# Kernel optimization log

Hardware: AMD Instinct MI355X
Metric: run time of the kernel (lower is better)

Reference implementation:

```python
import jax, jax.numpy as jnp
import numpy as np

B, T, D = 2, 2048, 2048
H = 8
KEY_DIM, VAL_DIM = 1024, 2048   # expand_k=0.5, expand_v=1.0
HK, HV = KEY_DIM // H, VAL_DIM // H
LOW_RANK = 16
GATE_NORM = 16.0
CHUNK = 64
HIDDEN = (D * 4 * 2 // 3 + 63) // 64 * 64  # 5504, exactly as GLUFFN.__init__
EPS = 1e-6


def rmsnorm(x, w):
    return x * jax.lax.rsqrt(jnp.mean(x * x, axis=-1, keepdims=True) + EPS) * w


def setup_inputs() -> dict:
    key = jax.random.key(0)
    ks = jax.random.split(key, 12)
    w = lambda k, s: jax.random.normal(k, s, jnp.float32) * 0.02
    return {
        "x": jax.random.normal(ks[0], (B, T, D), jnp.float32),
        "norm1_w": jnp.ones((D,), jnp.float32),
        "wq": w(ks[1], (D, KEY_DIM)),
        "wk": w(ks[2], (D, KEY_DIM)),
        "wv": w(ks[3], (D, VAL_DIM)),
        "gk_w1": w(ks[4], (D, LOW_RANK)),
        "gk_w2": w(ks[5], (LOW_RANK, KEY_DIM)),
        "gk_b": jnp.zeros((KEY_DIM,), jnp.float32),
        "wg": w(ks[6], (D, VAL_DIM)),
        "gnorm_w": jnp.ones((HV,), jnp.float32),
        "wo": w(ks[7], (VAL_DIM, D)),
        "ffn_norm_w": jnp.ones((D,), jnp.float32),
        "w_gate": w(ks[8], (D, HIDDEN)),
        "w_up": w(ks[9], (D, HIDDEN)),
        "w_down": w(ks[10], (HIDDEN, D)),
    }


def _gla(h, wq, wk, wv, gk_w1, gk_w2, gk_b, wg, gnorm_w, wo):
    # Gated linear attention, chunk-parallel form (fla-style):
    #   S_t = diag(exp(g_t)) S_{t-1} + k_t^T v_t ;  o_t = q_t S_t
    Bb, Tt, _ = h.shape
    nc = Tt // CHUNK

    def split(t, hd):  # [B,T,H*hd] -> [nc,B,H,CHUNK,hd]
        t = t.reshape(Bb, nc, CHUNK, H, hd)
        return jnp.transpose(t, (1, 0, 3, 2, 4))

    q = split(h @ wq, HK) * (HK ** -0.5)
    k = split(h @ wk, HK)
    v = split(h @ wv, HV)
    # low-rank forget gate, log-sigmoid scaled by gate_logit_normalizer=16
    g = split(jax.nn.log_sigmoid(h @ gk_w1 @ gk_w2 + gk_b) / GATE_NORM, HK)

    mask = jnp.tril(jnp.ones((CHUNK, CHUNK), jnp.float32))

    def step(S, inp):
        qc, kc, vc, gc = inp                       # [B,H,C,*]
        b = jnp.cumsum(gc, axis=-2)                # cumulative log-decay within chunk
        qe = qc * jnp.exp(b)
        A = jnp.einsum('bhik,bhjk->bhij', qe, kc * jnp.exp(-b)) * mask
        o = jnp.einsum('bhck,bhkv->bhcv', qe, S) + jnp.einsum('bhij,bhjv->bhiv', A, vc)
        bl = b[:, :, -1:, :]                       # decay to end of chunk
        S = jnp.exp(bl[:, :, 0, :])[..., None] * S + \
            jnp.einsum('bhck,bhcv->bhkv', kc * jnp.exp(bl - b), vc)
        return S, o

    S0 = jnp.zeros((Bb, H, HK, HV), h.dtype)
    _, o = jax.lax.scan(step, S0, (q, k, v, g))    # o: [nc,B,H,C,HV]
    o = jnp.transpose(o, (1, 0, 3, 2, 4)).reshape(Bb, Tt, H, HV)

    gate = (h @ wg).reshape(Bb, Tt, H, HV)
    # per-head RMSNorm + swish output gate (FusedRMSNormSwishGate)
    o = rmsnorm(o, gnorm_w) * gate * jax.nn.sigmoid(gate)
    return o.reshape(Bb, Tt, VAL_DIM) @ wo


def reference(x, norm1_w, wq, wk, wv, gk_w1, gk_w2, gk_b, wg, gnorm_w, wo,
              ffn_norm_w, w_gate, w_up, w_down):
    h = rmsnorm(x, norm1_w)
    x = x + _gla(h, wq, wk, wv, gk_w1, gk_w2, gk_b, wg, gnorm_w, wo)
    h2 = rmsnorm(x, ffn_norm_w)
    ffn = (jax.nn.silu(h2 @ w_gate) * (h2 @ w_up)) @ w_down  # GLUFFN, dropout=eval
    return x + ffn
```

## Files before the change

kernel.cpp:

```cpp
#include <hip/hip_runtime.h>

typedef unsigned short u16;
typedef __attribute__((ext_vector_type(8))) short bh8;
typedef __attribute__((ext_vector_type(4))) float f4;

__device__ __forceinline__ float bf2f(u16 u) {
  union { unsigned int i; float f; } x; x.i = ((unsigned int)u) << 16; return x.f;
}
__device__ __forceinline__ u16 f2bf(float f) {
  union { float f; unsigned int i; } x; x.f = f;
  unsigned int r = x.i + 0x7fffu + ((x.i >> 16) & 1u);
  return (u16)(r >> 16);
}
__device__ __forceinline__ f4 mfma16(bh8 a, bh8 b, f4 c) {
  return __builtin_amdgcn_mfma_f32_16x16x32_bf16(a, b, c, 0, 0, 0);
}
__device__ __forceinline__ void gload16(const void* g, void* l) {
  __builtin_amdgcn_global_load_lds(
      (const __attribute__((address_space(1))) void*)g,
      (__attribute__((address_space(3))) void*)l, 16, 0, 0);
}

__device__ __forceinline__ bh8 rd8(const u16* arr, int row, int col, int rowbytes) {
  return *(const bh8*)((const char*)arr + row * rowbytes + ((col * 2) ^ ((row & 7) << 4)));
}

__global__ __launch_bounds__(256)
void wtrans_k(const float* __restrict__ src, u16* __restrict__ dst, int R, int C,
              int rmul, int roff) {
  __shared__ float tile[32][33];
  int tx = threadIdx.x & 31, ty = threadIdx.x >> 5;
  int c0 = blockIdx.x * 32, r0 = blockIdx.y * 32;
#pragma unroll
  for (int yy = 0; yy < 32; yy += 8)
    tile[ty + yy][tx] = src[(size_t)(r0 + ty + yy) * C + c0 + tx];
  __syncthreads();
#pragma unroll
  for (int yy = 0; yy < 32; yy += 8)
    dst[(size_t)((c0 + ty + yy) * rmul + roff) * R + r0 + tx] = f2bf(tile[tx][ty + yy]);
}

__global__ __launch_bounds__(256)
void rmsnorm_k(const float* __restrict__ x, const float* __restrict__ w,
               u16* __restrict__ out) {
  int row = blockIdx.x, t = threadIdx.x;
  const float* xr = x + (size_t)row * 2048;
  float4 a = ((const float4*)xr)[t * 2];
  float4 b = ((const float4*)xr)[t * 2 + 1];
  float ss = a.x*a.x + a.y*a.y + a.z*a.z + a.w*a.w
           + b.x*b.x + b.y*b.y + b.z*b.z + b.w*b.w;
#pragma unroll
  for (int s = 32; s > 0; s >>= 1) ss += __shfl_xor(ss, s, 64);
  __shared__ float red[4];
  if ((t & 63) == 0) red[t >> 6] = ss;
  __syncthreads();
  float rr = rsqrtf((red[0] + red[1] + red[2] + red[3]) * (1.0f / 2048.0f) + 1e-6f);
  float v[8] = {a.x, a.y, a.z, a.w, b.x, b.y, b.z, b.w};
  int c0 = t * 8;
  u16* orow = out + (size_t)row * 2048 + c0;
#pragma unroll
  for (int j = 0; j < 8; ++j) orow[j] = f2bf(v[j] * rr * w[c0 + j]);
}

template <int EPI, int BN, typename OutT>
__global__ __launch_bounds__(256, 2)
void gemm2(const u16* __restrict__ A, const u16* __restrict__ Bt,
           OutT* __restrict__ C, void* __restrict__ aux, float scale,
           int M, int N, int K, int gx) {
  constexpr int SB = (BN == 256) ? 24576 : 16384;
  constexpr int NBS = (BN == 256) ? 4 : 2;
  constexpr int MB = (BN == 256) ? 8 : 4;
  __shared__ char lds[3 * SB];
  int t = threadIdx.x, lane = t & 63, w = t >> 6;
  int c_ = lane & 15, r_ = lane >> 4;
  int wm = (BN == 256) ? 0 : (w >> 1);
  int wn = (BN == 256) ? w : (w & 1);

  int nwg = gridDim.x;
  int wg = (blockIdx.x & 7) * (nwg >> 3) + (blockIdx.x >> 3);
  int gy = nwg / gx;
  int bx = wg / gy, by = wg % gy;
  int m0 = by * 128, n0 = bx * BN;

  const char* baseA[2];
#pragma unroll
  for (int h = 0; h < 2; ++h) {
    int p = h * 256 + t;
    int cc = p ^ ((p >> 3) & 7);
    baseA[h] = (const char*)A + ((size_t)(m0 + (cc >> 2)) * K + (cc & 3) * 8) * 2;
  }
  const char* baseB[NBS];
#pragma unroll
  for (int s = 0; s < NBS; ++s) {
    int p = s * 256 + t;
    int cc = p ^ ((p >> 3) & 7);
    baseB[s] = (const char*)Bt + ((size_t)(n0 + (cc >> 2)) * K + (cc & 3) * 8) * 2;
  }
  int offA[MB], offB[4];
#pragma unroll
  for (int mb = 0; mb < MB; ++mb) {
    int cc = (wm * 64 + mb * 16 + c_) * 4 + r_;
    offA[mb] = (cc ^ ((cc >> 3) & 7)) * 16;
  }
#pragma unroll
  for (int nb = 0; nb < 4; ++nb) {
    int cc = (wn * 64 + nb * 16 + c_) * 4 + r_;
    offB[nb] = (cc ^ ((cc >> 3) & 7)) * 16 + 8192;
  }
  int ldsW = w * 1024;

  f4 z4 = {0.f, 0.f, 0.f, 0.f};
  f4 acc[MB][4];
#pragma unroll
  for (int mb = 0; mb < MB; ++mb)
#pragma unroll
    for (int nb = 0; nb < 4; ++nb) acc[mb][nb] = z4;

  int NT = K >> 5;

#define STAGE(S, ko)                                                        \
  {                                                                         \
    _Pragma("unroll") for (int h = 0; h < 2; ++h)                           \
        gload16(baseA[h] + (ko), lds + (S) * SB + h * 4096 + ldsW);         \
    _Pragma("unroll") for (int s = 0; s < NBS; ++s)                         \
        gload16(baseB[s] + (ko), lds + (S) * SB + 8192 + s * 4096 + ldsW);  \
  }
#define WAIT_VM()                                                           \
  if (BN == 256) { asm volatile("s_waitcnt vmcnt(6)" ::: "memory"); }       \
  else { asm volatile("s_waitcnt vmcnt(4)" ::: "memory"); }
#define KTILE(S)                                                            \
  {                                                                         \
    bh8 afr[MB], bfr[4];                                                    \
    _Pragma("unroll") for (int nb = 0; nb < 4; ++nb)                        \
        bfr[nb] = *(const bh8*)(lds + (S) * SB + offB[nb]);                 \
    _Pragma("unroll") for (int mb = 0; mb < MB; ++mb)                       \
        afr[mb] = *(const bh8*)(lds + (S) * SB + offA[mb]);                 \
    int kts = kt + 2; if (kts >= NT) kts -= NT;                             \
    STAGE(((S) + 2) % 3, kts << 6);                                         \
    WAIT_VM();                                                              \
    __builtin_amdgcn_s_barrier();                                           \
    asm volatile("s_waitcnt lgkmcnt(0)" ::: "memory");                      \
    __builtin_amdgcn_sched_barrier(0);                                      \
    __builtin_amdgcn_s_setprio(1);                                          \
    _Pragma("unroll") for (int mb = 0; mb < MB; ++mb)                       \
        _Pragma("unroll") for (int nb = 0; nb < 4; ++nb)                    \
            acc[mb][nb] = mfma16(afr[mb], bfr[nb], acc[mb][nb]);            \
    __builtin_amdgcn_s_setprio(0);                                          \
    __builtin_amdgcn_sched_barrier(0);                                      \
    __builtin_amdgcn_s_barrier();                                           \
    asm volatile("" ::: "memory");                                          \
  }

  STAGE(0, 0);
  STAGE(1, 64);
  WAIT_VM();
  __builtin_amdgcn_s_barrier();
  asm volatile("" ::: "memory");

  int kt = 0;
  while (true) {
    KTILE(0); if (++kt == NT) break;
    KTILE(1); if (++kt == NT) break;
    KTILE(2); if (++kt == NT) break;
  }
  asm volatile("s_waitcnt vmcnt(0)" ::: "memory");
#undef KTILE
#undef WAIT_VM
#undef STAGE

  int rowBase = m0 + wm * 64;
#pragma unroll
  for (int mb = 0; mb < MB; ++mb) {
#pragma unroll
    for (int rr = 0; rr < 4; ++rr) {
      int row = rowBase + mb * 16 + r_ * 4 + rr;
#pragma unroll
      for (int nb = 0; nb < 4; ++nb) {
        int col = n0 + wn * 64 + nb * 16 + c_;
        float val = acc[mb][nb][rr];
        if (EPI == 1) {
          ((float*)C)[(size_t)row * N + col] = val + ((const float*)aux)[(size_t)row * N + col];
        } else if (EPI == 5) {
          if (col < 1024) ((u16*)C)[(size_t)row * 1024 + col] = f2bf(val * scale);
          else ((u16*)aux)[(size_t)row * 1024 + col - 1024] = f2bf(val);
        } else if (EPI == 4) {
          if (col < 2048) {
            int bb = row >> 11, t2 = row & 2047;
            int pan = ((bb << 5) + (t2 >> 6)) * 8 + (col >> 8);
            int ii = t2 & 63, vv = col & 255;
            *(u16*)((char*)C + (size_t)pan * 32768 + vv * 128 + ((ii * 2) ^ ((vv & 7) << 4)))
                = f2bf(val);
          } else {
            ((u16*)aux)[(size_t)row * 2048 + col - 2048] = f2bf(val);
          }
        } else if (EPI == 6) {
          float other = __shfl_xor(val, 1, 64);
          if (lane & 1) {
            float gv = other;
            ((u16*)C)[(size_t)row * 5504 + (col >> 1)] = f2bf(val * (gv / (1.f + expf(-gv))));
          }
        }
      }
    }
  }
}

__global__ __launch_bounds__(256)
void lowrank_k(const u16* __restrict__ h, const float* __restrict__ w1,
               const float* __restrict__ w2, const float* __restrict__ bias,
               float* __restrict__ g) {
  int row = blockIdx.x, t = threadIdx.x, lane = t & 63, wave = t >> 6;
  const u16* hr = h + (size_t)row * 2048;
  bh8 hv = *(const bh8*)&hr[t * 8];
  float p[16];
#pragma unroll
  for (int j = 0; j < 16; ++j) p[j] = 0.f;
#pragma unroll
  for (int kk = 0; kk < 8; ++kk) {
    float f = bf2f((u16)hv[kk]);
    const float* wrow = w1 + (size_t)(t * 8 + kk) * 16;
#pragma unroll
    for (int j = 0; j < 16; ++j) p[j] += f * wrow[j];
  }
#pragma unroll
  for (int j = 0; j < 16; ++j)
#pragma unroll
    for (int s = 32; s > 0; s >>= 1) p[j] += __shfl_xor(p[j], s, 64);
  __shared__ float gl[4][16];
  if (lane == 0) {
#pragma unroll
    for (int j = 0; j < 16; ++j) gl[wave][j] = p[j];
  }
  __syncthreads();
  float glow[16];
#pragma unroll
  for (int j = 0; j < 16; ++j) glow[j] = gl[0][j] + gl[1][j] + gl[2][j] + gl[3][j];
  float* grow = g + (size_t)row * 1024;
#pragma unroll
  for (int nn = 0; nn < 4; ++nn) {
    int n = nn * 256 + t;
    float z = bias[n];
#pragma unroll
    for (int j = 0; j < 16; ++j) z += glow[j] * w2[j * 1024 + n];
    float ls = fminf(z, 0.f) - log1pf(expf(-fabsf(z)));
    grow[n] = ls * (1.0f / 16.0f);
  }
}

__global__ __launch_bounds__(128)
void gprep_k(u16* __restrict__ q, u16* __restrict__ k, const float* __restrict__ g,
             u16* __restrict__ keT, float* __restrict__ ebl) {
  int bid = blockIdx.x;
  int h = bid & 7, bc = bid >> 3;
  int b = bc >> 5, c = bc & 31;
  int ch = threadIdx.x;
  size_t base = ((size_t)(b * 2048 + c * 64)) * 1024 + h * 128 + ch;
  char* keTp = (char*)keT + (size_t)bid * 16384 + ch * 128;
  int sw = (ch & 7) << 4;
  float bacc = 0.f;
  for (int i8 = 0; i8 < 8; ++i8) {
    u16 kp[8];
#pragma unroll
    for (int e = 0; e < 8; ++e) {
      size_t off = base + (size_t)(i8 * 8 + e) * 1024;
      bacc += g[off];
      float eb = __expf(bacc);
      float reb = __builtin_amdgcn_rcpf(eb);
      float qv = bf2f(q[off]), kv = bf2f(k[off]);
      q[off] = f2bf(qv * eb);
      u16 kev = f2bf(kv * reb);
      k[off] = kev;
      kp[e] = kev;
    }
    *(bh8*)(keTp + ((i8 * 16) ^ sw)) = *(const bh8*)kp;
  }
  ebl[(size_t)bid * 128 + ch] = __expf(bacc);
}

__global__ __launch_bounds__(256)
void gla_scan(const u16* __restrict__ qg, const u16* __restrict__ kg,
              const u16* __restrict__ keTg, const u16* __restrict__ vTg,
              const float* __restrict__ eblg, float* __restrict__ outp) {
  __shared__ u16 qeL[64 * 128];
  __shared__ u16 keL[64 * 128];
  __shared__ u16 kTL[128 * 64];
  __shared__ u16 vTL[64 * 64];
  __shared__ u16 AL[64 * 64];
  __shared__ u16 SbL[64 * 128];
  __shared__ float SfL[64][133];

  int t = threadIdx.x, lane = t & 63, w = t >> 6;
  int vb = blockIdx.x & 3, bh = blockIdx.x >> 2;
  int b = bh >> 3, h = bh & 7;
  int c_ = lane & 15, r_ = lane >> 4;
  f4 z4 = {0.f, 0.f, 0.f, 0.f};

  for (int i = t; i < 64 * 128; i += 256) SbL[i] = 0;
  for (int i = t; i < 64 * 133; i += 256) ((float*)SfL)[i] = 0.f;

  const char* qbase = (const char*)qg + (size_t)b * 2048 * 2048 + h * 256;
  const char* kbase = (const char*)kg + (size_t)b * 2048 * 2048 + h * 256;
  int rowoff = (t >> 4) * 2048 + (t & 15) * 16;
  int4 pq[4], pk[4], pkt[4], pvt[2];

#define LOADCH(cc)                                                              \
  {                                                                             \
    const char* qc = qbase + (size_t)(cc) * 64 * 2048;                          \
    const char* kc = kbase + (size_t)(cc) * 64 * 2048;                          \
    int panel_ = ((b * 32 + (cc)) * 8 + h);                                     \
    const char* ktc = (const char*)keTg + (size_t)panel_ * 16384;               \
    const char* vtc = (const char*)vTg + (size_t)panel_ * 32768 + vb * 8192;    \
    _Pragma("unroll")                                                           \
    for (int j = 0; j < 4; ++j) {                                               \
      pq[j] = *(const int4*)(qc + j * 16 * 2048 + rowoff);                      \
      pk[j] = *(const int4*)(kc + j * 16 * 2048 + rowoff);                      \
      pkt[j] = *(const int4*)(ktc + j * 4096 + t * 16);                         \
    }                                                                           \
    _Pragma("unroll")                                                           \
    for (int j = 0; j < 2; ++j) pvt[j] = *(const int4*)(vtc + j * 4096 + t * 16); \
  }

  LOADCH(0);
  for (int c = 0; c < 32; ++c) {
#pragma unroll
    for (int j = 0; j < 4; ++j) {
      int L = j * 4096 + t * 16;
      int d = (L & ~255) | ((L & 255) ^ (((L >> 8) & 7) << 4));
      *(int4*)((char*)qeL + d) = pq[j];
      *(int4*)((char*)keL + d) = pk[j];
      *(int4*)((char*)kTL + L) = pkt[j];
    }
#pragma unroll
    for (int j = 0; j < 2; ++j) *(int4*)((char*)vTL + j * 4096 + t * 16) = pvt[j];
    if (c < 31) LOADCH(c + 1);
    int panel = ((b * 32 + c) * 8 + h);
    float eblr[2][4];
#pragma unroll
    for (int kt = 0; kt < 2; ++kt)
#pragma unroll
      for (int r = 0; r < 4; ++r)
        eblr[kt][r] = eblg[(size_t)panel * 128 + w * 32 + kt * 16 + r_ * 4 + r];
    __syncthreads();

    f4 accA[4] = {z4, z4, z4, z4};
    f4 accS[2][4] = {{z4, z4, z4, z4}, {z4, z4, z4, z4}};
#pragma unroll
    for (int ks = 0; ks < 4; ++ks) {
      bh8 a = rd8(qeL, w * 16 + c_, ks * 32 + r_ * 8, 256);
#pragma unroll
      for (int n = 0; n < 4; ++n)
        accA[n] = mfma16(a, rd8(keL, n * 16 + c_, ks * 32 + r_ * 8, 256), accA[n]);
    }
#pragma unroll
    for (int ks = 0; ks < 2; ++ks) {
      bh8 bf_[4];
#pragma unroll
      for (int n = 0; n < 4; ++n) bf_[n] = rd8(vTL, n * 16 + c_, ks * 32 + r_ * 8, 128);
#pragma unroll
      for (int kt = 0; kt < 2; ++kt) {
        bh8 a = rd8(kTL, w * 32 + kt * 16 + c_, ks * 32 + r_ * 8, 128);
#pragma unroll
        for (int n = 0; n < 4; ++n) accS[kt][n] = mfma16(a, bf_[n], accS[kt][n]);
      }
    }
#pragma unroll
    for (int n = 0; n < 4; ++n)
#pragma unroll
      for (int r = 0; r < 4; ++r) {
        int i = w * 16 + r_ * 4 + r, j = n * 16 + c_;
        *(u16*)((char*)AL + i * 128 + ((j * 2) ^ ((i & 7) << 4))) =
            (j <= i) ? f2bf(accA[n][r]) : (u16)0;
      }
    __syncthreads();

    f4 acco[4] = {z4, z4, z4, z4};
#pragma unroll
    for (int ks = 0; ks < 4; ++ks) {
      bh8 a = rd8(qeL, w * 16 + c_, ks * 32 + r_ * 8, 256);
#pragma unroll
      for (int n = 0; n < 4; ++n)
        acco[n] = mfma16(a, rd8(SbL, n * 16 + c_, ks * 32 + r_ * 8, 256), acco[n]);
    }
#pragma unroll
    for (int ks = 0; ks < 2; ++ks) {
      bh8 a = rd8(AL, w * 16 + c_, ks * 32 + r_ * 8, 128);
#pragma unroll
      for (int n = 0; n < 4; ++n)
        acco[n] = mfma16(a, rd8(vTL, n * 16 + c_, ks * 32 + r_ * 8, 128), acco[n]);
    }
    {
      size_t obase = (size_t)(b * 2048 + c * 64 + w * 16 + r_ * 4) * 2048 + h * 256 + vb * 64;
#pragma unroll
      for (int n = 0; n < 4; ++n)
#pragma unroll
        for (int r = 0; r < 4; ++r)
          outp[obase + (size_t)r * 2048 + n * 16 + c_] = acco[n][r];
    }
    __syncthreads();

#pragma unroll
    for (int kt = 0; kt < 2; ++kt)
#pragma unroll
      for (int n = 0; n < 4; ++n)
#pragma unroll
        for (int r = 0; r < 4; ++r) {
          int kk = w * 32 + kt * 16 + r_ * 4 + r;
          int vcol = n * 16 + c_;
          float nv = eblr[kt][r] * (SfL[vcol][kk] + accS[kt][n][r]);
          SfL[vcol][kk] = nv;
          *(u16*)((char*)SbL + vcol * 256 + ((kk * 2) ^ ((vcol & 7) << 4))) = f2bf(nv);
        }
    __syncthreads();
  }
#undef LOADCH
}

__global__ __launch_bounds__(256)
void ogate_k(const float* __restrict__ o, const u16* __restrict__ gate,
             const float* __restrict__ gw, u16* __restrict__ og) {
  int tok = blockIdx.x, t = threadIdx.x;
  int head = t >> 5, l32 = t & 31, v0 = l32 * 8;
  size_t base = (size_t)tok * 2048 + head * 256 + v0;
  float4 a = *(const float4*)&o[base];
  float4 b = *(const float4*)&o[base + 4];
  float ov[8] = {a.x, a.y, a.z, a.w, b.x, b.y, b.z, b.w};
  float ss = 0.f;
#pragma unroll
  for (int j = 0; j < 8; ++j) ss += ov[j] * ov[j];
#pragma unroll
  for (int s = 16; s > 0; s >>= 1) ss += __shfl_xor(ss, s, 32);
  float rr = rsqrtf(ss * (1.0f / 256.0f) + 1e-6f);
#pragma unroll
  for (int j = 0; j < 8; ++j) {
    float gv = bf2f(gate[base + j]);
    float val = ov[j] * rr * gw[v0 + j];
    og[base + j] = f2bf(val * gv / (1.f + expf(-gv)));
  }
}

extern "C" void kernel_launch(void* const* d_in, const int* in_sizes, int n_in,
                              void* d_out, int out_size, void* d_ws, size_t ws_size,
                              hipStream_t stream) {
  (void)in_sizes; (void)n_in; (void)out_size; (void)ws_size;
  const float* x = (const float*)d_in[0];
  const float* n1w = (const float*)d_in[1];
  const float* wq = (const float*)d_in[2];
  const float* wk = (const float*)d_in[3];
  const float* wv = (const float*)d_in[4];
  const float* gw1 = (const float*)d_in[5];
  const float* gw2 = (const float*)d_in[6];
  const float* gb = (const float*)d_in[7];
  const float* wg = (const float*)d_in[8];
  const float* gnw = (const float*)d_in[9];
  const float* wo = (const float*)d_in[10];
  const float* fnw = (const float*)d_in[11];
  const float* wgate = (const float*)d_in[12];
  const float* wup = (const float*)d_in[13];
  const float* wdown = (const float*)d_in[14];
  float* out = (float*)d_out;

  char* ws = (char*)d_ws;
  size_t off = 0;
  auto alloc = [&](size_t bytes) { size_t p = off; off += (bytes + 255) & ~(size_t)255; return p; };
  u16* wqT = (u16*)(ws + alloc(2ull * 1024 * 2048));
  u16* wkT = (u16*)(ws + alloc(2ull * 1024 * 2048));
  u16* wvT = (u16*)(ws + alloc(2ull * 2048 * 2048));
  u16* wgT = (u16*)(ws + alloc(2ull * 2048 * 2048));
  u16* woT = (u16*)(ws + alloc(2ull * 2048 * 2048));
  u16* btGU = (u16*)(ws + alloc(2ull * 11008 * 2048));
  u16* wdT = (u16*)(ws + alloc(2ull * 2048 * 5504));
  u16* h_bf = (u16*)(ws + alloc(2ull * 4096 * 2048));
  u16* q_bf = (u16*)(ws + alloc(2ull * 4096 * 1024));
  u16* k_bf = (u16*)(ws + alloc(2ull * 4096 * 1024));
  u16* vT_g = (u16*)(ws + alloc(2ull * 4096 * 2048));
  u16* gate_bf = (u16*)(ws + alloc(2ull * 4096 * 2048));
  float* g_f = (float*)(ws + alloc(4ull * 4096 * 1024));
  float* o_f = (float*)(ws + alloc(4ull * 4096 * 2048));
  u16* mid = (u16*)(ws + alloc(2ull * 4096 * 5504));
  float* ebl_g = (float*)(ws + alloc(4ull * 512 * 128));
  u16* keT_g = h_bf;
  u16* og = h_bf;
  u16* h2 = q_bf;
  float* x2 = o_f;

  dim3 blk(256);
  wtrans_k<<<dim3(32, 64), blk, 0, stream>>>(wq, wqT, 2048, 1024, 1, 0);
  wtrans_k<<<dim3(32, 64), blk, 0, stream>>>(wk, wkT, 2048, 1024, 1, 0);
  wtrans_k<<<dim3(64, 64), blk, 0, stream>>>(wv, wvT, 2048, 2048, 1, 0);
  wtrans_k<<<dim3(64, 64), blk, 0, stream>>>(wg, wgT, 2048, 2048, 1, 0);
  wtrans_k<<<dim3(64, 64), blk, 0, stream>>>(wo, woT, 2048, 2048, 1, 0);
  wtrans_k<<<dim3(172, 64), blk, 0, stream>>>(wgate, btGU, 2048, 5504, 2, 0);
  wtrans_k<<<dim3(172, 64), blk, 0, stream>>>(wup, btGU, 2048, 5504, 2, 1);
  wtrans_k<<<dim3(64, 172), blk, 0, stream>>>(wdown, wdT, 5504, 2048, 1, 0);

  rmsnorm_k<<<4096, blk, 0, stream>>>(x, n1w, h_bf);

  gemm2<5, 128, u16><<<512, blk, 0, stream>>>(h_bf, wqT, q_bf, k_bf, 0.08838834764831845f,
                                              4096, 2048, 2048, 16);
  gemm2<4, 256, u16><<<512, blk, 0, stream>>>(h_bf, wvT, vT_g, gate_bf, 1.f,
                                              4096, 4096, 2048, 16);
  lowrank_k<<<4096, blk, 0, stream>>>(h_bf, gw1, gw2, gb, g_f);

  gprep_k<<<512, dim3(128), 0, stream>>>(q_bf, k_bf, g_f, keT_g, ebl_g);

  gla_scan<<<64, blk, 0, stream>>>(q_bf, k_bf, keT_g, vT_g, ebl_g, o_f);

  ogate_k<<<4096, blk, 0, stream>>>(o_f, gate_bf, gnw, og);

  gemm2<1, 128, float><<<512, blk, 0, stream>>>(og, woT, x2, (void*)x, 1.f,
                                                4096, 2048, 2048, 16);

  rmsnorm_k<<<4096, blk, 0, stream>>>(x2, fnw, h2);

  gemm2<6, 256, u16><<<1376, blk, 0, stream>>>(h2, btGU, mid, nullptr, 1.f,
                                               4096, 11008, 2048, 43);
  gemm2<1, 128, float><<<512, blk, 0, stream>>>(mid, wdT, out, x2, 1.f,
                                                4096, 2048, 5504, 16);
}
```

Baseline: 1.017 ms.

## Software-pipeline LDS fragment loads in GEMM and drop the 256-wide tile variant

The GEMM main loop now double-buffers its register fragments: it reads the next k-tile's A/B fragments from LDS while issuing MFMAs on the current ones, with the loop unrolled six ways to alternate buffers. The BN=256 variant is removed, so every GEMM uses 128x128 tiles and the grids for the V/gate and gate/up GEMMs double in size. The aim is to hide LDS read latency behind MFMA work. In exchange it adds register pressure, and the smaller tiles re-read more A/B data from global memory.

```diff
diff --git a/kernel.cpp b/kernel.cpp
--- a/kernel.cpp
+++ b/kernel.cpp
@@ -62,25 +62,22 @@
   for (int j = 0; j < 8; ++j) orow[j] = f2bf(v[j] * rr * w[c0 + j]);
 }
 
-template <int EPI, int BN, typename OutT>
+template <int EPI, typename OutT>
 __global__ __launch_bounds__(256, 2)
 void gemm2(const u16* __restrict__ A, const u16* __restrict__ Bt,
            OutT* __restrict__ C, void* __restrict__ aux, float scale,
            int M, int N, int K, int gx) {
-  constexpr int SB = (BN == 256) ? 24576 : 16384;
-  constexpr int NBS = (BN == 256) ? 4 : 2;
-  constexpr int MB = (BN == 256) ? 8 : 4;
+  constexpr int SB = 16384;
   __shared__ char lds[3 * SB];
   int t = threadIdx.x, lane = t & 63, w = t >> 6;
   int c_ = lane & 15, r_ = lane >> 4;
-  int wm = (BN == 256) ? 0 : (w >> 1);
-  int wn = (BN == 256) ? w : (w & 1);
+  int wm = w >> 1, wn = w & 1;
 
   int nwg = gridDim.x;
   int wg = (blockIdx.x & 7) * (nwg >> 3) + (blockIdx.x >> 3);
   int gy = nwg / gx;
   int bx = wg / gy, by = wg % gy;
-  int m0 = by * 128, n0 = bx * BN;
+  int m0 = by * 128, n0 = bx * 128;
 
   const char* baseA[2];
 #pragma unroll
@@ -89,16 +86,16 @@
     int cc = p ^ ((p >> 3) & 7);
     baseA[h] = (const char*)A + ((size_t)(m0 + (cc >> 2)) * K + (cc & 3) * 8) * 2;
   }
-  const char* baseB[NBS];
-#pragma unroll
-  for (int s = 0; s < NBS; ++s) {
+  const char* baseB[2];
+#pragma unroll
+  for (int s = 0; s < 2; ++s) {
     int p = s * 256 + t;
     int cc = p ^ ((p >> 3) & 7);
     baseB[s] = (const char*)Bt + ((size_t)(n0 + (cc >> 2)) * K + (cc & 3) * 8) * 2;
   }
-  int offA[MB], offB[4];
-#pragma unroll
-  for (int mb = 0; mb < MB; ++mb) {
+  int offA[4], offB[4];
+#pragma unroll
+  for (int mb = 0; mb < 4; ++mb) {
     int cc = (wm * 64 + mb * 16 + c_) * 4 + r_;
     offA[mb] = (cc ^ ((cc >> 3) & 7)) * 16;
   }
@@ -110,41 +107,37 @@
   int ldsW = w * 1024;
 
   f4 z4 = {0.f, 0.f, 0.f, 0.f};
-  f4 acc[MB][4];
-#pragma unroll
-  for (int mb = 0; mb < MB; ++mb)
+  f4 acc[4][4];
+#pragma unroll
+  for (int mb = 0; mb < 4; ++mb)
 #pragma unroll
     for (int nb = 0; nb < 4; ++nb) acc[mb][nb] = z4;
 
   int NT = K >> 5;
+  bh8 fa[2][4], fb[2][4];
 
 #define STAGE(S, ko)                                                        \
   {                                                                         \
     _Pragma("unroll") for (int h = 0; h < 2; ++h)                           \
         gload16(baseA[h] + (ko), lds + (S) * SB + h * 4096 + ldsW);         \
-    _Pragma("unroll") for (int s = 0; s < NBS; ++s)                         \
+    _Pragma("unroll") for (int s = 0; s < 2; ++s)                           \
         gload16(baseB[s] + (ko), lds + (S) * SB + 8192 + s * 4096 + ldsW);  \
   }
-#define WAIT_VM()                                                           \
-  if (BN == 256) { asm volatile("s_waitcnt vmcnt(6)" ::: "memory"); }       \
-  else { asm volatile("s_waitcnt vmcnt(4)" ::: "memory"); }
-#define KTILE(S)                                                            \
+#define KTILE(S, P)                                                         \
   {                                                                         \
-    bh8 afr[MB], bfr[4];                                                    \
+    int kts = kt + 2; if (kts >= NT) kts -= NT;                             \
+    STAGE((((S) + 2) % 3), (kts << 6));                                     \
+    asm volatile("s_waitcnt vmcnt(4)" ::: "memory");                        \
+    __builtin_amdgcn_s_barrier();                                           \
     _Pragma("unroll") for (int nb = 0; nb < 4; ++nb)                        \
-        bfr[nb] = *(const bh8*)(lds + (S) * SB + offB[nb]);                 \
-    _Pragma("unroll") for (int mb = 0; mb < MB; ++mb)                       \
-        afr[mb] = *(const bh8*)(lds + (S) * SB + offA[mb]);                 \
-    int kts = kt + 2; if (kts >= NT) kts -= NT;                             \
-    STAGE(((S) + 2) % 3, kts << 6);                                         \
-    WAIT_VM();                                                              \
-    __builtin_amdgcn_s_barrier();                                           \
-    asm volatile("s_waitcnt lgkmcnt(0)" ::: "memory");                      \
+        fb[(P) ^ 1][nb] = *(const bh8*)(lds + ((((S) + 1) % 3) * SB) + offB[nb]); \
+    _Pragma("unroll") for (int mb = 0; mb < 4; ++mb)                        \
+        fa[(P) ^ 1][mb] = *(const bh8*)(lds + ((((S) + 1) % 3) * SB) + offA[mb]); \
     __builtin_amdgcn_sched_barrier(0);                                      \
     __builtin_amdgcn_s_setprio(1);                                          \
-    _Pragma("unroll") for (int mb = 0; mb < MB; ++mb)                       \
+    _Pragma("unroll") for (int mb = 0; mb < 4; ++mb)                        \
         _Pragma("unroll") for (int nb = 0; nb < 4; ++nb)                    \
-            acc[mb][nb] = mfma16(afr[mb], bfr[nb], acc[mb][nb]);            \
+            acc[mb][nb] = mfma16(fa[P][mb], fb[P][nb], acc[mb][nb]);        \
     __builtin_amdgcn_s_setprio(0);                                          \
     __builtin_amdgcn_sched_barrier(0);                                      \
     __builtin_amdgcn_s_barrier();                                           \
@@ -153,24 +146,29 @@
 
   STAGE(0, 0);
   STAGE(1, 64);
-  WAIT_VM();
+  asm volatile("s_waitcnt vmcnt(4)" ::: "memory");
   __builtin_amdgcn_s_barrier();
-  asm volatile("" ::: "memory");
+#pragma unroll
+  for (int nb = 0; nb < 4; ++nb) fb[0][nb] = *(const bh8*)(lds + offB[nb]);
+#pragma unroll
+  for (int mb = 0; mb < 4; ++mb) fa[0][mb] = *(const bh8*)(lds + offA[mb]);
 
   int kt = 0;
   while (true) {
-    KTILE(0); if (++kt == NT) break;
-    KTILE(1); if (++kt == NT) break;
-    KTILE(2); if (++kt == NT) break;
+    KTILE(0, 0); if (++kt == NT) break;
+    KTILE(1, 1); if (++kt == NT) break;
+    KTILE(2, 0); if (++kt == NT) break;
+    KTILE(0, 1); if (++kt == NT) break;
+    KTILE(1, 0); if (++kt == NT) break;
+    KTILE(2, 1); if (++kt == NT) break;
   }
   asm volatile("s_waitcnt vmcnt(0)" ::: "memory");
 #undef KTILE
-#undef WAIT_VM
 #undef STAGE
 
   int rowBase = m0 + wm * 64;
 #pragma unroll
-  for (int mb = 0; mb < MB; ++mb) {
+  for (int mb = 0; mb < 4; ++mb) {
 #pragma unroll
     for (int rr = 0; rr < 4; ++rr) {
       int row = rowBase + mb * 16 + r_ * 4 + rr;
@@ -495,10 +493,10 @@
 
   rmsnorm_k<<<4096, blk, 0, stream>>>(x, n1w, h_bf);
 
-  gemm2<5, 128, u16><<<512, blk, 0, stream>>>(h_bf, wqT, q_bf, k_bf, 0.08838834764831845f,
-                                              4096, 2048, 2048, 16);
-  gemm2<4, 256, u16><<<512, blk, 0, stream>>>(h_bf, wvT, vT_g, gate_bf, 1.f,
-                                              4096, 4096, 2048, 16);
+  gemm2<5, u16><<<512, blk, 0, stream>>>(h_bf, wqT, q_bf, k_bf, 0.08838834764831845f,
+                                         4096, 2048, 2048, 16);
+  gemm2<4, u16><<<1024, blk, 0, stream>>>(h_bf, wvT, vT_g, gate_bf, 1.f,
+                                          4096, 4096, 2048, 32);
   lowrank_k<<<4096, blk, 0, stream>>>(h_bf, gw1, gw2, gb, g_f);
 
   gprep_k<<<512, dim3(128), 0, stream>>>(q_bf, k_bf, g_f, keT_g, ebl_g);
@@ -507,13 +505,13 @@
 
   ogate_k<<<4096, blk, 0, stream>>>(o_f, gate_bf, gnw, og);
 
-  gemm2<1, 128, float><<<512, blk, 0, stream>>>(og, woT, x2, (void*)x, 1.f,
-                                                4096, 2048, 2048, 16);
+  gemm2<1, float><<<512, blk, 0, stream>>>(og, woT, x2, (void*)x, 1.f,
+                                           4096, 2048, 2048, 16);
 
   rmsnorm_k<<<4096, blk, 0, stream>>>(x2, fnw, h2);
 
-  gemm2<6, 256, u16><<<1376, blk, 0, stream>>>(h2, btGU, mid, nullptr, 1.f,
-                                               4096, 11008, 2048, 43);
-  gemm2<1, 128, float><<<512, blk, 0, stream>>>(mid, wdT, out, x2, 1.f,
-                                                4096, 2048, 5504, 16);
-}
+  gemm2<6, u16><<<2752, blk, 0, stream>>>(h2, btGU, mid, nullptr, 1.f,
+                                          4096, 11008, 2048, 86);
+  gemm2<1, float><<<512, blk, 0, stream>>>(mid, wdT, out, x2, 1.f,
+                                           4096, 2048, 5504, 16);
+}
```

Measured after the change: 1.049 ms. 3.1% more time.
